# Kernel optimization log

Hardware: AMD Instinct MI355X
Metric: run time of the kernel (lower is better)

Reference implementation:

```python
import jax, jax.numpy as jnp
import numpy as np

N_NODES = 100000
N_EDGES = 3200000
D_IN = 256      # encoder_dim feeding gnn_1
D_GNN = 256     # decoder_output_dim * 4
N_CLUSTER = 4
SIGMA = 0.5
V = 1.0


def setup_inputs() -> dict:
    key = jax.random.key(0)
    ks = jax.random.split(key, 16)
    f = lambda k, shp: jax.random.normal(k, shp, dtype=jnp.float32)
    inp = {
        "encoded_input_data": f(ks[0], (N_NODES, D_IN)),
        "tra1": f(ks[1], (N_NODES, D_GNN)),
        "tra2": f(ks[2], (N_NODES, D_GNN)),
        "tra3": f(ks[3], (N_NODES, D_GNN)),
        "z":    f(ks[4], (N_NODES, D_GNN)),
        "edge_row": jax.random.randint(ks[5], (N_EDGES,), 0, N_NODES, dtype=jnp.int32),
        "edge_col": jax.random.randint(ks[6], (N_EDGES,), 0, N_NODES, dtype=jnp.int32),
        "edge_vals": jax.random.uniform(ks[7], (N_EDGES,), dtype=jnp.float32),
        "W1": f(ks[8], (D_IN, D_GNN)) * (1.0 / np.sqrt(D_IN)),
        "W2": f(ks[9], (D_GNN, D_GNN)) * (1.0 / np.sqrt(D_GNN)),
        "W3": f(ks[10], (D_GNN, D_GNN)) * (1.0 / np.sqrt(D_GNN)),
        "W4": f(ks[11], (D_GNN, D_GNN)) * (1.0 / np.sqrt(D_GNN)),
        "W5": f(ks[12], (D_GNN, N_CLUSTER)) * (1.0 / np.sqrt(D_GNN)),
        "cluster": f(ks[13], (N_CLUSTER, D_GNN)),
    }
    return inp


def _spmm(row, col, vals, x):
    # sparse adj (COO) @ x : gather source rows, scale, scatter-add to dest rows
    return jax.ops.segment_sum(vals[:, None] * x[col], row, num_segments=N_NODES)


def _gnn(x, W, row, col, vals, active=True):
    out = _spmm(row, col, vals, x @ W)
    return jax.nn.relu(out) if active else out


def reference(encoded_input_data, tra1, tra2, tra3, z,
              edge_row, edge_col, edge_vals,
              W1, W2, W3, W4, W5, cluster):
    r, c, vals = edge_row, edge_col, edge_vals
    h = _gnn(encoded_input_data, W1, r, c, vals)
    h = _gnn((1 - SIGMA) * h + SIGMA * tra1, W2, r, c, vals)
    h = _gnn((1 - SIGMA) * h + SIGMA * tra2, W3, r, c, vals)
    h = _gnn((1 - SIGMA) * h + SIGMA * tra3, W4, r, c, vals)
    h = _gnn((1 - SIGMA) * h + SIGMA * z, W5, r, c, vals, active=False)
    predict = jax.nn.softmax(h, axis=1)  # [N, n_cluster]

    # student-t soft assignment: ||z_i - mu_j||^2 expanded to avoid [N,K,D] blowup
    dist2 = (jnp.sum(z * z, axis=1, keepdims=True)
             - 2.0 * (z @ cluster.T)
             + jnp.sum(cluster * cluster, axis=1)[None, :])
    q = 1.0 / (1.0 + dist2 / V)
    q = q ** ((V + 1.0) / 2.0)
    q = q / jnp.sum(q, axis=1, keepdims=True)

    return jnp.concatenate([predict, q], axis=1)  # [N, 2*n_cluster]
```

## Files before the change

kernel.cpp:

```cpp
#include <hip/hip_runtime.h>

#define NN 100000
#define NE 3200000
#define DD 256
#define KC 4
#define MPAD 100096
#define NBUK ((NN + 255) >> 8)
#define B2 782
#define EPB 4096
#define NS2 (NBUK * B2)
#define INV15 (1.0f / 32767.0f)

typedef _Float16 f16x8 __attribute__((ext_vector_type(8)));
typedef float f32x4 __attribute__((ext_vector_type(4)));


__global__ __launch_bounds__(256) void k_h2(const int* __restrict__ row,
                                            int* __restrict__ h2) {
    __shared__ int cnt[NBUK];
    const int b = blockIdx.x;
    for (int i = threadIdx.x; i < NBUK; i += 256) cnt[i] = 0;
    __syncthreads();
    const int e0 = b * EPB;
    const int e1 = min(e0 + EPB, NE);
    for (int e = e0 + (int)threadIdx.x; e < e1; e += 256)
        atomicAdd(&cnt[row[e] >> 8], 1);
    __syncthreads();
    for (int i = threadIdx.x; i < NBUK; i += 256) h2[i * B2 + b] = cnt[i];
}

__global__ __launch_bounds__(256) void k_scan1g(const int* __restrict__ in,
                                                int* __restrict__ out,
                                                int* __restrict__ bsum, int n) {
    __shared__ int s[256];
    const int t = threadIdx.x;
    const int base = blockIdx.x * 1024 + t * 4;
    int v[4];
    int sum = 0;
#pragma unroll
    for (int i = 0; i < 4; ++i) {
        v[i] = (base + i < n) ? in[base + i] : 0;
        sum += v[i];
    }
    s[t] = sum;
    __syncthreads();
    for (int off = 1; off < 256; off <<= 1) {
        int x = (t >= off) ? s[t - off] : 0;
        __syncthreads();
        s[t] += x;
        __syncthreads();
    }
    int run = (t > 0) ? s[t - 1] : 0;
#pragma unroll
    for (int i = 0; i < 4; ++i) {
        if (base + i < n) out[base + i] = run;
        run += v[i];
    }
    if (t == 255) bsum[blockIdx.x] = s[255];
}

__global__ void k_scan2(int* __restrict__ bsum, int nb) {
    if (threadIdx.x == 0 && blockIdx.x == 0) {
        int run = 0;
        for (int i = 0; i < nb; ++i) {
            int c = bsum[i];
            bsum[i] = run;
            run += c;
        }
    }
}

__global__ __launch_bounds__(256) void k_scan3g(int* __restrict__ out,
                                                const int* __restrict__ bsum,
                                                int n, int total) {
    int i = blockIdx.x * 256 + threadIdx.x;
    if (i < n)
        out[i] += bsum[i >> 10];
    else if (i == n)
        out[n] = total;
}

__global__ __launch_bounds__(256) void k_bin(const int* __restrict__ row,
                                             const int* __restrict__ col,
                                             const float* __restrict__ val,
                                             const int* __restrict__ s2cur,
                                             int2* __restrict__ recs) {
    __shared__ int cur[NBUK];
    const int b = blockIdx.x;
    for (int i = threadIdx.x; i < NBUK; i += 256) cur[i] = s2cur[i * B2 + b];
    __syncthreads();
    const int e0 = b * EPB;
    const int e1 = min(e0 + EPB, NE);
    for (int e = e0 + (int)threadIdx.x; e < e1; e += 256) {
        const int r = row[e];
        const unsigned v15 = (unsigned)(val[e] * 32767.f + 0.5f);
        const unsigned packed = (v15 << 17) | (unsigned)col[e];
        const int p = atomicAdd(&cur[r >> 8], 1);
        int2 rec;
        rec.x = (int)packed;
        rec.y = r;
        recs[p] = rec;
    }
}

__global__ __launch_bounds__(256) void k_place(const int2* __restrict__ recs,
                                               const int* __restrict__ s2cur,
                                               int* __restrict__ offs,
                                               unsigned* __restrict__ edges) {
    __shared__ int cnt[256];
    __shared__ int s[256];
    __shared__ int lcur[256];
    const int b = blockIdx.x;
    const int t = threadIdx.x;
    const int lo = b << 8;
    const int hi = min(lo + 256, NN);
    const int nr = hi - lo;
    const int base = s2cur[b * B2];
    const int end = s2cur[(b + 1) * B2];
    cnt[t] = 0;
    __syncthreads();
    for (int i = base + t; i < end; i += 256) atomicAdd(&cnt[recs[i].y - lo], 1);
    __syncthreads();
    s[t] = cnt[t];
    __syncthreads();
    for (int off = 1; off < 256; off <<= 1) {
        int x = (t >= off) ? s[t - off] : 0;
        __syncthreads();
        s[t] += x;
        __syncthreads();
    }
    const int excl = (t > 0) ? s[t - 1] : 0;
    if (t < nr) offs[lo + t] = base + excl;
    if (b == NBUK - 1 && t == 0) offs[NN] = NE;
    lcur[t] = base + excl;
    __syncthreads();
    for (int i = base + t; i < end; i += 256) {
        const int2 rec = recs[i];
        const int p = atomicAdd(&lcur[rec.y - lo], 1);
        edges[p] = (unsigned)rec.x;
    }
}


__global__ __launch_bounds__(256) void k_cvtX(const float* __restrict__ in,
                                              _Float16* __restrict__ out) {
    const size_t base = ((size_t)blockIdx.x * 256 + threadIdx.x) * 8;
    if (base >= (size_t)NN * DD) return;
    f32x4 v0 = __builtin_nontemporal_load(reinterpret_cast<const f32x4*>(in + base));
    f32x4 v1 = __builtin_nontemporal_load(reinterpret_cast<const f32x4*>(in + base + 4));
    f16x8 o;
    o[0] = (_Float16)v0[0]; o[1] = (_Float16)v0[1]; o[2] = (_Float16)v0[2]; o[3] = (_Float16)v0[3];
    o[4] = (_Float16)v1[0]; o[5] = (_Float16)v1[1]; o[6] = (_Float16)v1[2]; o[7] = (_Float16)v1[3];
    *reinterpret_cast<f16x8*>(out + base) = o;
}

__global__ __launch_bounds__(256) void k_cvtW(const float* __restrict__ W1,
                                              const float* __restrict__ W2,
                                              const float* __restrict__ W3,
                                              const float* __restrict__ W4,
                                              _Float16* __restrict__ Wt) {
    __shared__ float s[32][33];
    const float* W = (blockIdx.z == 0) ? W1 : (blockIdx.z == 1) ? W2 : (blockIdx.z == 2) ? W3 : W4;
    _Float16* o = Wt + (size_t)blockIdx.z * DD * DD;
    const int bk = blockIdx.x * 32;
    const int bn = blockIdx.y * 32;
    const int tx = threadIdx.x & 31, ty = threadIdx.x >> 5;
    for (int r = ty; r < 32; r += 8) s[r][tx] = W[(size_t)(bk + r) * DD + bn + tx];
    __syncthreads();
    for (int r = ty; r < 32; r += 8) o[(size_t)(bn + r) * DD + bk + tx] = (_Float16)s[tx][r];
}


__device__ __forceinline__ void load_lds16(const void* g, void* l) {
    __builtin_amdgcn_global_load_lds((const __attribute__((address_space(1))) void*)g,
                                     (__attribute__((address_space(3))) void*)l, 16, 0, 0);
}

__global__ __launch_bounds__(512, 4) void k_gemm_h(const _Float16* __restrict__ X,
                                                   const _Float16* __restrict__ Wt,
                                                   _Float16* __restrict__ Y) {
    __shared__ __align__(16) char lds[49152];
    char* const Albase = lds;
    char* const Blbase = lds + 16384;

    const int tid = threadIdx.x;
    const int lane = tid & 63;
    const int wid = tid >> 6;
    const int wr = wid >> 2;
    const int wc = wid & 3;
    const int bm = blockIdx.x * 128;

    const int aoffl = wid * 1024 + lane * 16;
    const int arw = aoffl >> 6;
    const int acb = (aoffl & 63) ^ (((arw >> 1) & 3) << 4);
    const char* const Asrc0 = (const char*)X + ((size_t)(bm + arw) * DD) * 2 + acb;
    char* const Adst0 = Albase + wid * 1024;

    const int boffl0 = wid * 1024 + lane * 16;
    const int brw0 = boffl0 >> 6;
    const int bcb0 = (boffl0 & 63) ^ (((brw0 >> 1) & 3) << 4);
    const char* const Bsrc0 = (const char*)Wt + ((size_t)brw0 * DD) * 2 + bcb0;
    const int boffl1 = 8192 + wid * 1024 + lane * 16;
    const int brw1 = boffl1 >> 6;
    const int bcb1 = (boffl1 & 63) ^ (((brw1 >> 1) & 3) << 4);
    const char* const Bsrc1 = (const char*)Wt + ((size_t)brw1 * DD) * 2 + bcb1;
    char* const Bdst0 = Blbase + wid * 1024;
    char* const Bdst1 = Blbase + 8192 + wid * 1024;

    int aro[4], bro[4];
#pragma unroll
    for (int m = 0; m < 4; ++m) {
        const int r = wr * 64 + m * 16 + (lane & 15);
        aro[m] = r * 64 + ((((lane >> 4) * 16)) ^ (((r >> 1) & 3) << 4));
    }
#pragma unroll
    for (int n = 0; n < 4; ++n) {
        const int r = wc * 64 + n * 16 + (lane & 15);
        bro[n] = r * 64 + ((((lane >> 4) * 16)) ^ (((r >> 1) & 3) << 4));
    }

    f32x4 acc[4][4];
#pragma unroll
    for (int m = 0; m < 4; ++m)
#pragma unroll
        for (int n = 0; n < 4; ++n) acc[m][n] = (f32x4){0.f, 0.f, 0.f, 0.f};

    load_lds16(Asrc0, Adst0);
    load_lds16(Bsrc0, Bdst0);
    load_lds16(Bsrc1, Bdst1);
    __syncthreads();

    for (int kt = 0; kt < 8; ++kt) {
        const int cur = kt & 1;
        if (kt < 7) {
            const size_t kb = (size_t)(kt + 1) * 32 * 2;
            load_lds16(Asrc0 + kb, Adst0 + (cur ^ 1) * 8192);
            load_lds16(Bsrc0 + kb, Bdst0 + (cur ^ 1) * 16384);
            load_lds16(Bsrc1 + kb, Bdst1 + (cur ^ 1) * 16384);
        }
        const char* Ab = Albase + cur * 8192;
        const char* Bb = Blbase + cur * 16384;
        f16x8 af[4], bf[4];
#pragma unroll
        for (int m = 0; m < 4; ++m) af[m] = *reinterpret_cast<const f16x8*>(Ab + aro[m]);
#pragma unroll
        for (int n = 0; n < 4; ++n) bf[n] = *reinterpret_cast<const f16x8*>(Bb + bro[n]);
#pragma unroll
        for (int m = 0; m < 4; ++m)
#pragma unroll
            for (int n = 0; n < 4; ++n)
                acc[m][n] = __builtin_amdgcn_mfma_f32_16x16x32_f16(af[m], bf[n], acc[m][n], 0, 0, 0);
        __syncthreads();
    }

#pragma unroll
    for (int m = 0; m < 4; ++m) {
        const int row = bm + wr * 64 + m * 16 + (lane >> 4) * 4;
#pragma unroll
        for (int n = 0; n < 4; ++n) {
            const int col = wc * 64 + n * 16 + (lane & 15);
#pragma unroll
            for (int j = 0; j < 4; ++j)
                Y[(size_t)(row + j) * DD + col] = (_Float16)acc[m][n][j];
        }
    }
}


__global__ __launch_bounds__(256) void k_spmm_h(const int* __restrict__ offs,
                                                const unsigned* __restrict__ edges,
                                                const _Float16* __restrict__ Y,
                                                const float* __restrict__ blend,
                                                _Float16* __restrict__ Xout) {
    const int row = blockIdx.x * 4 + (threadIdx.x >> 6);
    if (row >= NN) return;
    const int lane = threadIdx.x & 63;
    const int half = lane >> 5;
    const int sub = lane & 31;
    const int e0 = offs[row], e1 = offs[row + 1];
    float acc[8] = {};
    int e = e0 + half;
    for (; e + 6 < e1; e += 8) {
        const unsigned u0 = edges[e], u1 = edges[e + 2], u2 = edges[e + 4], u3 = edges[e + 6];
        const float v0 = (float)(u0 >> 17) * INV15;
        const float v1 = (float)(u1 >> 17) * INV15;
        const float v2 = (float)(u2 >> 17) * INV15;
        const float v3 = (float)(u3 >> 17) * INV15;
        const f16x8 y0 = *reinterpret_cast<const f16x8*>(Y + ((size_t)(u0 & 0x1FFFFu) << 8) + sub * 8);
        const f16x8 y1 = *reinterpret_cast<const f16x8*>(Y + ((size_t)(u1 & 0x1FFFFu) << 8) + sub * 8);
        const f16x8 y2 = *reinterpret_cast<const f16x8*>(Y + ((size_t)(u2 & 0x1FFFFu) << 8) + sub * 8);
        const f16x8 y3 = *reinterpret_cast<const f16x8*>(Y + ((size_t)(u3 & 0x1FFFFu) << 8) + sub * 8);
#pragma unroll
        for (int j = 0; j < 8; ++j)
            acc[j] += v0 * (float)y0[j] + v1 * (float)y1[j] + v2 * (float)y2[j] + v3 * (float)y3[j];
    }
    for (; e < e1; e += 2) {
        const unsigned u = edges[e];
        const float v = (float)(u >> 17) * INV15;
        const f16x8 y = *reinterpret_cast<const f16x8*>(Y + ((size_t)(u & 0x1FFFFu) << 8) + sub * 8);
#pragma unroll
        for (int j = 0; j < 8; ++j) acc[j] += v * (float)y[j];
    }
#pragma unroll
    for (int j = 0; j < 8; ++j) acc[j] += __shfl_xor(acc[j], 32);
    if (half == 0) {
        const size_t bi = (size_t)row * DD + sub * 8;
        const f32x4 t0 = __builtin_nontemporal_load(reinterpret_cast<const f32x4*>(blend + bi));
        const f32x4 t1 = __builtin_nontemporal_load(reinterpret_cast<const f32x4*>(blend + bi + 4));
        f16x8 o;
        o[0] = (_Float16)(0.5f * fmaxf(acc[0], 0.f) + 0.5f * t0[0]);
        o[1] = (_Float16)(0.5f * fmaxf(acc[1], 0.f) + 0.5f * t0[1]);
        o[2] = (_Float16)(0.5f * fmaxf(acc[2], 0.f) + 0.5f * t0[2]);
        o[3] = (_Float16)(0.5f * fmaxf(acc[3], 0.f) + 0.5f * t0[3]);
        o[4] = (_Float16)(0.5f * fmaxf(acc[4], 0.f) + 0.5f * t1[0]);
        o[5] = (_Float16)(0.5f * fmaxf(acc[5], 0.f) + 0.5f * t1[1]);
        o[6] = (_Float16)(0.5f * fmaxf(acc[6], 0.f) + 0.5f * t1[2]);
        o[7] = (_Float16)(0.5f * fmaxf(acc[7], 0.f) + 0.5f * t1[3]);
        *reinterpret_cast<f16x8*>(Xout + bi) = o;
    }
}

__global__ __launch_bounds__(256) void k_spmm_last(const int* __restrict__ offs,
                                                   const unsigned* __restrict__ edges,
                                                   const _Float16* __restrict__ Y,
                                                   const float* __restrict__ z,
                                                   const float* __restrict__ W5,
                                                   const float* __restrict__ cl,
                                                   float* __restrict__ Y5,
                                                   float* __restrict__ out) {
    const int row = blockIdx.x * 4 + (threadIdx.x >> 6);
    if (row >= NN) return;
    const int lane = threadIdx.x & 63;
    const int half = lane >> 5;
    const int sub = lane & 31;
    const int e0 = offs[row], e1 = offs[row + 1];
    float acc[8] = {};
    int e = e0 + half;
    for (; e + 6 < e1; e += 8) {
        const unsigned u0 = edges[e], u1 = edges[e + 2], u2 = edges[e + 4], u3 = edges[e + 6];
        const float v0 = (float)(u0 >> 17) * INV15;
        const float v1 = (float)(u1 >> 17) * INV15;
        const float v2 = (float)(u2 >> 17) * INV15;
        const float v3 = (float)(u3 >> 17) * INV15;
        const f16x8 y0 = *reinterpret_cast<const f16x8*>(Y + ((size_t)(u0 & 0x1FFFFu) << 8) + sub * 8);
        const f16x8 y1 = *reinterpret_cast<const f16x8*>(Y + ((size_t)(u1 & 0x1FFFFu) << 8) + sub * 8);
        const f16x8 y2 = *reinterpret_cast<const f16x8*>(Y + ((size_t)(u2 & 0x1FFFFu) << 8) + sub * 8);
        const f16x8 y3 = *reinterpret_cast<const f16x8*>(Y + ((size_t)(u3 & 0x1FFFFu) << 8) + sub * 8);
#pragma unroll
        for (int j = 0; j < 8; ++j)
            acc[j] += v0 * (float)y0[j] + v1 * (float)y1[j] + v2 * (float)y2[j] + v3 * (float)y3[j];
    }
    for (; e < e1; e += 2) {
        const unsigned u = edges[e];
        const float v = (float)(u >> 17) * INV15;
        const f16x8 y = *reinterpret_cast<const f16x8*>(Y + ((size_t)(u & 0x1FFFFu) << 8) + sub * 8);
#pragma unroll
        for (int j = 0; j < 8; ++j) acc[j] += v * (float)y[j];
    }
#pragma unroll
    for (int j = 0; j < 8; ++j) acc[j] += __shfl_xor(acc[j], 32);
    if (half == 0) {
        const size_t bi = (size_t)row * DD + sub * 8;
        const f32x4 z0 = __builtin_nontemporal_load(reinterpret_cast<const f32x4*>(z + bi));
        const f32x4 z1 = __builtin_nontemporal_load(reinterpret_cast<const f32x4*>(z + bi + 4));
        const float zb[8] = {z0[0], z0[1], z0[2], z0[3], z1[0], z1[1], z1[2], z1[3]};
        float p[4] = {0.f, 0.f, 0.f, 0.f};
        float zz = 0.f;
#pragma unroll
        for (int j = 0; j < 8; ++j) {
            const float b = 0.5f * fmaxf(acc[j], 0.f) + 0.5f * zb[j];
            const f32x4 w = *reinterpret_cast<const f32x4*>(W5 + (size_t)(sub * 8 + j) * KC);
            p[0] += b * w[0];
            p[1] += b * w[1];
            p[2] += b * w[2];
            p[3] += b * w[3];
            zz += zb[j] * zb[j];
        }
        float dot[4] = {0.f, 0.f, 0.f, 0.f}, cc[4] = {0.f, 0.f, 0.f, 0.f};
#pragma unroll
        for (int c2 = 0; c2 < 4; ++c2) {
            const f32x4 c40 = *reinterpret_cast<const f32x4*>(cl + (size_t)c2 * DD + sub * 8);
            const f32x4 c41 = *reinterpret_cast<const f32x4*>(cl + (size_t)c2 * DD + sub * 8 + 4);
            dot[c2] = zb[0] * c40[0] + zb[1] * c40[1] + zb[2] * c40[2] + zb[3] * c40[3] +
                      zb[4] * c41[0] + zb[5] * c41[1] + zb[6] * c41[2] + zb[7] * c41[3];
            cc[c2] = c40[0] * c40[0] + c40[1] * c40[1] + c40[2] * c40[2] + c40[3] * c40[3] +
                     c41[0] * c41[0] + c41[1] * c41[1] + c41[2] * c41[2] + c41[3] * c41[3];
        }
#pragma unroll
        for (int o = 16; o; o >>= 1) {
            zz += __shfl_xor(zz, o);
#pragma unroll
            for (int c2 = 0; c2 < 4; ++c2) {
                p[c2] += __shfl_xor(p[c2], o);
                dot[c2] += __shfl_xor(dot[c2], o);
                cc[c2] += __shfl_xor(cc[c2], o);
            }
        }
        if (sub == 0) {
            *reinterpret_cast<f32x4*>(Y5 + (size_t)row * KC) = (f32x4){p[0], p[1], p[2], p[3]};
            float q[4], s = 0.f;
#pragma unroll
            for (int c2 = 0; c2 < 4; ++c2) {
                const float d2 = zz - 2.f * dot[c2] + cc[c2];
                q[c2] = 1.f / (1.f + d2);
                s += q[c2];
            }
            const float inv = 1.f / s;
            *reinterpret_cast<f32x4*>(out + (size_t)row * 8 + 4) =
                (f32x4){q[0] * inv, q[1] * inv, q[2] * inv, q[3] * inv};
        }
    }
}


__device__ inline float wred(float v) {
#pragma unroll
    for (int o = 32; o; o >>= 1) v += __shfl_down(v, o);
    return v;
}

__global__ __launch_bounds__(256) void k_sm5(const int* __restrict__ offs,
                                             const unsigned* __restrict__ edges,
                                             const float* __restrict__ Y5,
                                             float* __restrict__ out) {
    const int row = blockIdx.x * 4 + (threadIdx.x >> 6);
    if (row >= NN) return;
    const int lane = threadIdx.x & 63;
    const int e0 = offs[row], e1 = offs[row + 1];
    float ax = 0.f, ay = 0.f, az = 0.f, aw = 0.f;
    for (int e = e0 + lane; e < e1; e += 64) {
        const unsigned u = edges[e];
        const float v = (float)(u >> 17) * INV15;
        const f32x4 y = *reinterpret_cast<const f32x4*>(Y5 + (size_t)(u & 0x1FFFFu) * KC);
        ax += v * y[0];
        ay += v * y[1];
        az += v * y[2];
        aw += v * y[3];
    }
    ax = wred(ax);
    ay = wred(ay);
    az = wred(az);
    aw = wred(aw);
    if (lane == 0) {
        float m = fmaxf(fmaxf(ax, ay), fmaxf(az, aw));
        float ex = __expf(ax - m), ey = __expf(ay - m), ez = __expf(az - m), ew = __expf(aw - m);
        float inv = 1.f / (ex + ey + ez + ew);
        *reinterpret_cast<f32x4*>(out + (size_t)row * 8) =
            (f32x4){ex * inv, ey * inv, ez * inv, ew * inv};
    }
}


extern "C" void kernel_launch(void* const* d_in, const int* in_sizes, int n_in,
                              void* d_out, int out_size, void* d_ws, size_t ws_size,
                              hipStream_t stream) {
    const float* enc = (const float*)d_in[0];
    const float* tra1 = (const float*)d_in[1];
    const float* tra2 = (const float*)d_in[2];
    const float* tra3 = (const float*)d_in[3];
    const float* z = (const float*)d_in[4];
    const int* erow = (const int*)d_in[5];
    const int* ecol = (const int*)d_in[6];
    const float* evals = (const float*)d_in[7];
    const float* W1 = (const float*)d_in[8];
    const float* W2 = (const float*)d_in[9];
    const float* W3 = (const float*)d_in[10];
    const float* W4 = (const float*)d_in[11];
    const float* W5 = (const float*)d_in[12];
    const float* cluster = (const float*)d_in[13];
    float* out = (float*)d_out;

    char* ws = (char*)d_ws;
    size_t off = 0;
    auto take = [&](size_t bytes) -> void* {
        void* p = ws + off;
        off = (off + bytes + 255) & ~(size_t)255;
        return p;
    };
    int* offs = (int*)take((size_t)(NN + 1) * 4);
    int* h2 = (int*)take((size_t)NS2 * 4);
    int* s2cur = (int*)take((size_t)(NS2 + 1) * 4);
    int* bsum = (int*)take(4096);
    int2* recs = (int2*)take((size_t)NE * 8);
    unsigned* edges = (unsigned*)take((size_t)NE * 4);
    _Float16* Xa = (_Float16*)take((size_t)MPAD * DD * 2);
    _Float16* Xb = (_Float16*)take((size_t)MPAD * DD * 2);
    _Float16* Wt = (_Float16*)take((size_t)4 * DD * DD * 2);
    float* Y5 = (float*)take((size_t)NN * KC * 4);

    k_h2<<<B2, 256, 0, stream>>>(erow, h2);
    const int nb2 = (NS2 + 1023) / 1024;
    k_scan1g<<<nb2, 256, 0, stream>>>(h2, s2cur, bsum, NS2);
    k_scan2<<<1, 64, 0, stream>>>(bsum, nb2);
    k_scan3g<<<(NS2 + 256) / 256, 256, 0, stream>>>(s2cur, bsum, NS2, NE);
    k_bin<<<B2, 256, 0, stream>>>(erow, ecol, evals, s2cur, recs);
    k_place<<<NBUK, 256, 0, stream>>>(recs, s2cur, offs, edges);

    k_cvtX<<<(NN * DD / 8 + 255) / 256, 256, 0, stream>>>(enc, Xa);
    k_cvtW<<<dim3(8, 8, 4), 256, 0, stream>>>(W1, W2, W3, W4, Wt);

    const int gb = MPAD / 128;
    const int rb = NN / 4;

    k_gemm_h<<<gb, 512, 0, stream>>>(Xa, Wt + 0 * DD * DD, Xb);
    k_spmm_h<<<rb, 256, 0, stream>>>(offs, edges, Xb, tra1, Xa);

    k_gemm_h<<<gb, 512, 0, stream>>>(Xa, Wt + 1 * DD * DD, Xb);
    k_spmm_h<<<rb, 256, 0, stream>>>(offs, edges, Xb, tra2, Xa);

    k_gemm_h<<<gb, 512, 0, stream>>>(Xa, Wt + 2 * DD * DD, Xb);
    k_spmm_h<<<rb, 256, 0, stream>>>(offs, edges, Xb, tra3, Xa);

    k_gemm_h<<<gb, 512, 0, stream>>>(Xa, Wt + 3 * DD * DD, Xb);
    k_spmm_last<<<rb, 256, 0, stream>>>(offs, edges, Xb, z, W5, cluster, Y5, out);

    k_sm5<<<rb, 256, 0, stream>>>(offs, edges, Y5, out);
}
```

Before: 1.194 ms.

## Fuse fp32 input conversion and relu-blend into GEMM A-tile loading

Removes the standalone fp32-to-fp16 conversion kernel by having the first GEMM read fp32 encoder input directly and convert it while staging the A tile. The relu and sigma-blend with tra1/2/3 move from the SpMM epilogue into the next GEMM's A-load, so SpMM writes raw fp16 aggregates. A loads switch from async global_load_lds to register loads with a manual LDS store after the MFMAs, which may weaken latency hiding. The relu is now applied to an fp16-rounded value rather than the fp32 accumulator, a small precision change.

```diff
diff --git a/kernel.cpp b/kernel.cpp
--- a/kernel.cpp
+++ b/kernel.cpp
@@ -142,18 +142,6 @@
 }
 
 
-__global__ __launch_bounds__(256) void k_cvtX(const float* __restrict__ in,
-                                              _Float16* __restrict__ out) {
-    const size_t base = ((size_t)blockIdx.x * 256 + threadIdx.x) * 8;
-    if (base >= (size_t)NN * DD) return;
-    f32x4 v0 = __builtin_nontemporal_load(reinterpret_cast<const f32x4*>(in + base));
-    f32x4 v1 = __builtin_nontemporal_load(reinterpret_cast<const f32x4*>(in + base + 4));
-    f16x8 o;
-    o[0] = (_Float16)v0[0]; o[1] = (_Float16)v0[1]; o[2] = (_Float16)v0[2]; o[3] = (_Float16)v0[3];
-    o[4] = (_Float16)v1[0]; o[5] = (_Float16)v1[1]; o[6] = (_Float16)v1[2]; o[7] = (_Float16)v1[3];
-    *reinterpret_cast<f16x8*>(out + base) = o;
-}
-
 __global__ __launch_bounds__(256) void k_cvtW(const float* __restrict__ W1,
                                               const float* __restrict__ W2,
                                               const float* __restrict__ W3,
@@ -176,7 +164,9 @@
                                      (__attribute__((address_space(3))) void*)l, 16, 0, 0);
 }
 
-__global__ __launch_bounds__(512, 4) void k_gemm_h(const _Float16* __restrict__ X,
+__global__ __launch_bounds__(512, 4) void k_gemm_f(const float* __restrict__ X1f,
+                                                   const _Float16* __restrict__ X1h,
+                                                   const float* __restrict__ X2f,
                                                    const _Float16* __restrict__ Wt,
                                                    _Float16* __restrict__ Y) {
     __shared__ __align__(16) char lds[49152];
@@ -190,11 +180,11 @@
     const int wc = wid & 3;
     const int bm = blockIdx.x * 128;
 
-    const int aoffl = wid * 1024 + lane * 16;
-    const int arw = aoffl >> 6;
-    const int acb = (aoffl & 63) ^ (((arw >> 1) & 3) << 4);
-    const char* const Asrc0 = (const char*)X + ((size_t)(bm + arw) * DD) * 2 + acb;
-    char* const Adst0 = Albase + wid * 1024;
+    const int arow = tid >> 2;
+    const int ac16 = tid & 3;
+    const int adst = arow * 64 + ((ac16 * 16) ^ (((arow >> 1) & 3) << 4));
+    const int agr = min(bm + arow, NN - 1);
+    const size_t abase = (size_t)agr * DD + ac16 * 8;
 
     const int boffl0 = wid * 1024 + lane * 16;
     const int brw0 = boffl0 >> 6;
@@ -219,22 +209,50 @@
         bro[n] = r * 64 + ((((lane >> 4) * 16)) ^ (((r >> 1) & 3) << 4));
     }
 
+    auto loadA = [&](int kt) -> f16x8 {
+        f16x8 a;
+        const size_t idx = abase + (size_t)kt * 32;
+        if (X1f) {
+            const f32x4 u0 = *reinterpret_cast<const f32x4*>(X1f + idx);
+            const f32x4 u1 = *reinterpret_cast<const f32x4*>(X1f + idx + 4);
+#pragma unroll
+            for (int j = 0; j < 4; ++j) {
+                a[j] = (_Float16)u0[j];
+                a[4 + j] = (_Float16)u1[j];
+            }
+        } else {
+            const f16x8 g = *reinterpret_cast<const f16x8*>(X1h + idx);
+            const f32x4 t0 = *reinterpret_cast<const f32x4*>(X2f + idx);
+            const f32x4 t1 = *reinterpret_cast<const f32x4*>(X2f + idx + 4);
+#pragma unroll
+            for (int j = 0; j < 4; ++j) {
+                a[j] = (_Float16)(0.5f * fmaxf((float)g[j], 0.f) + 0.5f * t0[j]);
+                a[4 + j] = (_Float16)(0.5f * fmaxf((float)g[4 + j], 0.f) + 0.5f * t1[j]);
+            }
+        }
+        return a;
+    };
+
     f32x4 acc[4][4];
 #pragma unroll
     for (int m = 0; m < 4; ++m)
 #pragma unroll
         for (int n = 0; n < 4; ++n) acc[m][n] = (f32x4){0.f, 0.f, 0.f, 0.f};
 
-    load_lds16(Asrc0, Adst0);
-    load_lds16(Bsrc0, Bdst0);
-    load_lds16(Bsrc1, Bdst1);
+    {
+        f16x8 a0 = loadA(0);
+        *reinterpret_cast<f16x8*>(Albase + adst) = a0;
+        load_lds16(Bsrc0, Bdst0);
+        load_lds16(Bsrc1, Bdst1);
+    }
     __syncthreads();
 
     for (int kt = 0; kt < 8; ++kt) {
         const int cur = kt & 1;
+        f16x8 aNext;
         if (kt < 7) {
+            aNext = loadA(kt + 1);
             const size_t kb = (size_t)(kt + 1) * 32 * 2;
-            load_lds16(Asrc0 + kb, Adst0 + (cur ^ 1) * 8192);
             load_lds16(Bsrc0 + kb, Bdst0 + (cur ^ 1) * 16384);
             load_lds16(Bsrc1 + kb, Bdst1 + (cur ^ 1) * 16384);
         }
@@ -250,6 +268,9 @@
 #pragma unroll
             for (int n = 0; n < 4; ++n)
                 acc[m][n] = __builtin_amdgcn_mfma_f32_16x16x32_f16(af[m], bf[n], acc[m][n], 0, 0, 0);
+        if (kt < 7) {
+            *reinterpret_cast<f16x8*>(Albase + (cur ^ 1) * 8192 + adst) = aNext;
+        }
         __syncthreads();
     }
 
@@ -270,7 +291,6 @@
 __global__ __launch_bounds__(256) void k_spmm_h(const int* __restrict__ offs,
                                                 const unsigned* __restrict__ edges,
                                                 const _Float16* __restrict__ Y,
-                                                const float* __restrict__ blend,
                                                 _Float16* __restrict__ Xout) {
     const int row = blockIdx.x * 4 + (threadIdx.x >> 6);
     if (row >= NN) return;
@@ -304,19 +324,10 @@
 #pragma unroll
     for (int j = 0; j < 8; ++j) acc[j] += __shfl_xor(acc[j], 32);
     if (half == 0) {
-        const size_t bi = (size_t)row * DD + sub * 8;
-        const f32x4 t0 = __builtin_nontemporal_load(reinterpret_cast<const f32x4*>(blend + bi));
-        const f32x4 t1 = __builtin_nontemporal_load(reinterpret_cast<const f32x4*>(blend + bi + 4));
         f16x8 o;
-        o[0] = (_Float16)(0.5f * fmaxf(acc[0], 0.f) + 0.5f * t0[0]);
-        o[1] = (_Float16)(0.5f * fmaxf(acc[1], 0.f) + 0.5f * t0[1]);
-        o[2] = (_Float16)(0.5f * fmaxf(acc[2], 0.f) + 0.5f * t0[2]);
-        o[3] = (_Float16)(0.5f * fmaxf(acc[3], 0.f) + 0.5f * t0[3]);
-        o[4] = (_Float16)(0.5f * fmaxf(acc[4], 0.f) + 0.5f * t1[0]);
-        o[5] = (_Float16)(0.5f * fmaxf(acc[5], 0.f) + 0.5f * t1[1]);
-        o[6] = (_Float16)(0.5f * fmaxf(acc[6], 0.f) + 0.5f * t1[2]);
-        o[7] = (_Float16)(0.5f * fmaxf(acc[7], 0.f) + 0.5f * t1[3]);
-        *reinterpret_cast<f16x8*>(Xout + bi) = o;
+#pragma unroll
+        for (int j = 0; j < 8; ++j) o[j] = (_Float16)acc[j];
+        *reinterpret_cast<f16x8*>(Xout + (size_t)row * DD + sub * 8) = o;
     }
 }
 
@@ -496,22 +507,21 @@
     k_bin<<<B2, 256, 0, stream>>>(erow, ecol, evals, s2cur, recs);
     k_place<<<NBUK, 256, 0, stream>>>(recs, s2cur, offs, edges);
 
-    k_cvtX<<<(NN * DD / 8 + 255) / 256, 256, 0, stream>>>(enc, Xa);
     k_cvtW<<<dim3(8, 8, 4), 256, 0, stream>>>(W1, W2, W3, W4, Wt);
 
     const int gb = MPAD / 128;
     const int rb = NN / 4;
 
-    k_gemm_h<<<gb, 512, 0, stream>>>(Xa, Wt + 0 * DD * DD, Xb);
-    k_spmm_h<<<rb, 256, 0, stream>>>(offs, edges, Xb, tra1, Xa);
-
-    k_gemm_h<<<gb, 512, 0, stream>>>(Xa, Wt + 1 * DD * DD, Xb);
-    k_spmm_h<<<rb, 256, 0, stream>>>(offs, edges, Xb, tra2, Xa);
-
-    k_gemm_h<<<gb, 512, 0, stream>>>(Xa, Wt + 2 * DD * DD, Xb);
-    k_spmm_h<<<rb, 256, 0, stream>>>(offs, edges, Xb, tra3, Xa);
-
-    k_gemm_h<<<gb, 512, 0, stream>>>(Xa, Wt + 3 * DD * DD, Xb);
+    k_gemm_f<<<gb, 512, 0, stream>>>(enc, nullptr, nullptr, Wt + 0 * DD * DD, Xb);
+    k_spmm_h<<<rb, 256, 0, stream>>>(offs, edges, Xb, Xa);
+
+    k_gemm_f<<<gb, 512, 0, stream>>>(nullptr, Xa, tra1, Wt + 1 * DD * DD, Xb);
+    k_spmm_h<<<rb, 256, 0, stream>>>(offs, edges, Xb, Xa);
+
+    k_gemm_f<<<gb, 512, 0, stream>>>(nullptr, Xa, tra2, Wt + 2 * DD * DD, Xb);
+    k_spmm_h<<<rb, 256, 0, stream>>>(offs, edges, Xb, Xa);
+
+    k_gemm_f<<<gb, 512, 0, stream>>>(nullptr, Xa, tra3, Wt + 3 * DD * DD, Xb);
     k_spmm_last<<<rb, 256, 0, stream>>>(offs, edges, Xb, z, W5, cluster, Y5, out);
 
     k_sm5<<<rb, 256, 0, stream>>>(offs, edges, Y5, out);
```

Measured after the change: 1.260 ms. 1.06x slower.
